# Kernel tuning notes

Hardware: AMD Instinct MI355X
Metric: run time of the kernel (lower is better)

Reference implementation:

```python
import jax, jax.numpy as jnp
import numpy as np

EPS = 1e-6


def _dwconv3x3(x, k):
    # x: [B,C,H,W], k: [C,1,3,3] depthwise kernel (OIHW with feature_group_count=C)
    return jax.lax.conv_general_dilated(
        x, k, window_strides=(1, 1), padding='SAME',
        dimension_numbers=('NCHW', 'OIHW', 'NCHW'),
        feature_group_count=x.shape[1])


def setup_inputs() -> dict:
    key = jax.random.key(0)
    ks = jax.random.split(key, 10)
    B, C, H, W, E = 8, 128, 128, 128, 4
    s = 0.02
    return {
        'x': jax.random.normal(ks[0], (B, C, H, W), jnp.float32),
        'prompt': jax.random.normal(ks[1], (B, C), jnp.float32),
        'gamma': jnp.ones((C,), jnp.float32),
        'beta': jnp.zeros((C,), jnp.float32),
        'rw': jax.random.normal(ks[2], (2 * C, E), jnp.float32) * s,
        'rb': jnp.zeros((E,), jnp.float32),
        'w1': jax.random.normal(ks[3], (E, C, C), jnp.float32) * s,
        'b1': jnp.zeros((E, C), jnp.float32),
        'dw': jax.random.normal(ks[4], (E, C, 1, 3, 3), jnp.float32) * s,
        'bdw': jnp.zeros((E, C), jnp.float32),
        'w2': jax.random.normal(ks[5], (E, C, C), jnp.float32) * s,
        'b2': jnp.zeros((E, C), jnp.float32),
        'pw': jax.random.normal(ks[6], (C, C), jnp.float32) * s,
        'pb': jnp.zeros((C,), jnp.float32),
    }


def reference(x, prompt, gamma, beta, rw, rb, w1, b1, dw, bdw, w2, b2, pw, pb):
    B, C, H, W = x.shape
    E = rb.shape[0]
    topk = 2

    # LayerNorm over channel dim (applied on last axis after permute in torch)
    mu = x.mean(axis=1, keepdims=True)
    var = x.var(axis=1, keepdims=True)
    x_in = (x - mu) * jax.lax.rsqrt(var + EPS)
    x_in = x_in * gamma[None, :, None, None] + beta[None, :, None, None]

    # Router: global avg pooled feature + prompt -> softmax -> top-k
    feat_avg = x_in.mean(axis=(2, 3))                        # [B,C]
    logits = jnp.concatenate([feat_avg, prompt], axis=1) @ rw + rb  # [B,E]
    probs = jax.nn.softmax(logits, axis=-1)
    weights, indices = jax.lax.top_k(probs, topk)            # [B,topk]

    # Per-sample gate over experts: g[b,e] = sum_k weights[b,k] * (indices[b,k]==e)
    gate = jnp.einsum('bk,bke->be', weights, jax.nn.one_hot(indices, E, dtype=x.dtype))

    # Dense all-expert compute (as in the original masked implementation)
    y = jnp.einsum('bchw,eoc->ebohw', x_in, w1) + b1[:, None, :, None, None]  # [E,B,C,H,W]
    y = jax.vmap(_dwconv3x3, in_axes=(0, 0))(y, dw) + bdw[:, None, :, None, None]
    y = jax.nn.gelu(y, approximate=False)
    y = jnp.einsum('ebchw,eoc->ebohw', y, w2) + b2[:, None, :, None, None]

    out = jnp.einsum('ebchw,be->bchw', y, gate)
    proj = jnp.einsum('bchw,oc->bohw', out, pw) + pb[None, :, None, None]
    return x + proj
```

## Files before the change

### kernel.cpp

```cpp
#include <hip/hip_runtime.h>
#include <hip/hip_bf16.h>

#define BB 8
#define CC 128
#define HH 128
#define WW 128
#define HW (HH*WW)
#define EE 4
#define EPSL 1e-6f
#define PT1 8
#define LNP 128

typedef __attribute__((ext_vector_type(8))) short bf16x8;
typedef __attribute__((ext_vector_type(4))) float f32x4;

__device__ inline float b2f(unsigned short u){
  union { unsigned int i; float f; } v; v.i = ((unsigned int)u)<<16; return v.f;
}
__device__ inline unsigned short f2b(float f){
  union { float f; unsigned int i; } v; v.f = f;
  unsigned int x = v.i;
  return (unsigned short)((x + 0x7fffu + ((x>>16)&1u)) >> 16);
}
__device__ inline int swz(int px, int cbyte){
  return cbyte ^ ((((px)&7) ^ (((px)>>3)&3)) << 4);
}

__global__ __launch_bounds__(128) void k_ln(
    const float* __restrict__ x, const float* __restrict__ gamma,
    const float* __restrict__ beta, unsigned short* __restrict__ xin) {
  int b = blockIdx.y;
  int p0 = blockIdx.x*LNP;
  int tid = threadIdx.x;
  const float* xb = x + (size_t)b*CC*HW + p0 + tid;
  float s=0.f, s2=0.f;
  for (int c=0;c<CC;c++){ float v = xb[(size_t)c*HW]; s+=v; s2+=v*v; }
  float mu = s*(1.f/CC);
  float var = s2*(1.f/CC) - mu*mu;
  float rs = rsqrtf(var + EPSL);

  __shared__ unsigned short tile[LNP][CC+8];
  for (int c0=0;c0<CC;c0+=8){
    union { bf16x8 v; unsigned short s[8]; } pk;
    #pragma unroll
    for (int j=0;j<8;j++){
      float v = (xb[(size_t)(c0+j)*HW]-mu)*rs*gamma[c0+j]+beta[c0+j];
      pk.s[j]=f2b(v);
    }
    *(bf16x8*)&tile[tid][c0] = pk.v;
  }
  __syncthreads();
  unsigned short* xo = xin + ((size_t)b*HW + p0)*CC;
  #pragma unroll
  for (int it=0; it<16; ++it){
    int i = it*LNP + tid;
    int pr = i>>4, ck = (i&15)*8;
    *(bf16x8*)(xo + (size_t)i*8) = *(bf16x8*)&tile[pr][ck];
  }
}

__global__ __launch_bounds__(256) void k_feat(
    const unsigned short* __restrict__ xin, float* __restrict__ feat_sum) {
  int b = blockIdx.y;
  int g = blockIdx.x;
  int tid = threadIdx.x;
  int cg = (tid & 15) * 8;
  int po = tid >> 4;
  __shared__ float lfeat[CC];
  for (int c=tid;c<CC;c+=256) lfeat[c]=0.f;
  __syncthreads();
  const unsigned short* base = xin + ((size_t)b*HW + (size_t)g*128)*CC + cg;
  float acc[8] = {};
  #pragma unroll
  for (int i=0;i<8;i++){
    bf16x8 v = *(const bf16x8*)(base + (size_t)(i*16+po)*CC);
    #pragma unroll
    for (int j=0;j<8;j++) acc[j] += b2f((unsigned short)v[j]);
  }
  #pragma unroll
  for (int j=0;j<8;j++) atomicAdd(&lfeat[cg+j], acc[j]);
  __syncthreads();
  if (tid < CC) atomicAdd(&feat_sum[b*CC+tid], lfeat[tid]);
}

__global__ __launch_bounds__(256) void k_router(
    const float* __restrict__ feat_sum, const float* __restrict__ prompt,
    const float* __restrict__ rw, const float* __restrict__ rb,
    const float* __restrict__ b2, const float* __restrict__ pw,
    const float* __restrict__ pb,
    int* __restrict__ eidx, float* __restrict__ wgt, float* __restrict__ bias_out) {
  __shared__ float logits[BB][EE];
  __shared__ float gate[BB][EE];
  __shared__ float cb[BB][CC];
  int t = threadIdx.x;
  if (t < BB*EE) {
    int b = t/EE, e = t%EE;
    float acc = rb[e];
    for (int c=0;c<CC;c++) acc += (feat_sum[b*CC+c]*(1.f/HW))*rw[c*EE+e];
    for (int c=0;c<CC;c++) acc += prompt[b*CC+c]*rw[(CC+c)*EE+e];
    logits[b][e]=acc;
  }
  __syncthreads();
  if (t < BB) {
    int b=t;
    float m=-1e30f;
    for(int e=0;e<EE;e++) m=fmaxf(m,logits[b][e]);
    float s=0.f, pr[EE];
    for(int e=0;e<EE;e++){ pr[e]=__expf(logits[b][e]-m); s+=pr[e]; }
    for(int e=0;e<EE;e++){ pr[e]/=s; gate[b][e]=0.f; }
    int i1=0; for(int e=1;e<EE;e++) if (pr[e]>pr[i1]) i1=e;
    int i2=-1; for(int e=0;e<EE;e++){ if(e==i1) continue; if(i2<0||pr[e]>pr[i2]) i2=e; }
    eidx[b*2]=i1; eidx[b*2+1]=i2;
    wgt[b*2]=pr[i1]; wgt[b*2+1]=pr[i2];
    gate[b][i1]=pr[i1]; gate[b][i2]=pr[i2];
  }
  __syncthreads();
  for (int i=t;i<BB*CC;i+=256){
    int b=i/CC, c=i%CC;
    float a=0.f;
    for(int e=0;e<EE;e++) a += gate[b][e]*b2[e*CC+c];
    cb[b][c]=a;
  }
  __syncthreads();
  for (int i=t;i<BB*CC;i+=256){
    int b=i/CC, o=i%CC;
    float a=pb[o];
    for (int c=0;c<CC;c++) a += pw[o*CC+c]*cb[b][c];
    bias_out[b*CC+o]=a;
  }
}

__global__ __launch_bounds__(128) void k_prep(
    const float* __restrict__ pw, const float* __restrict__ w2,
    const float* __restrict__ w1,
    unsigned short* __restrict__ w2p, unsigned short* __restrict__ w1b){
  int eo = blockIdx.x; int e = eo/CC, o = eo%CC;
  int c = threadIdx.x;
  float a=0.f;
  for (int m=0;m<CC;m++) a += pw[o*CC+m]*w2[((size_t)e*CC+m)*CC+c];
  w2p[((size_t)e*CC+o)*CC+c] = f2b(a);
  w1b[((size_t)e*CC+o)*CC+c] = f2b(w1[((size_t)e*CC+o)*CC+c]);
}

__global__ __launch_bounds__(256) void k_scalew2(
    const unsigned short* __restrict__ w2p, const int* __restrict__ eidx,
    const float* __restrict__ wgt, unsigned short* __restrict__ w2s){
  int bk = blockIdx.y;
  int e = eidx[bk]; float wv = wgt[bk];
  int i = blockIdx.x*256 + threadIdx.x;
  const unsigned short* src = w2p + (size_t)e*CC*CC;
  w2s[(size_t)bk*CC*CC + i] = f2b(wv * b2f(src[i]));
}

__global__ __launch_bounds__(256) void k_gemm1(
    const unsigned short* __restrict__ xin, const unsigned short* __restrict__ w1b,
    const float* __restrict__ b1, const int* __restrict__ eidx,
    unsigned short* __restrict__ t1) {
  int bk = blockIdx.y; int b = bk>>1; int e = eidx[bk];
  int wave = threadIdx.x>>6, lane = threadIdx.x&63;
  int lr = lane&15, lg = lane>>4;
  int ob = wave*32;
  const unsigned short* Ae = w1b + (size_t)e*CC*CC;
  bf16x8 A[2][4];
  #pragma unroll
  for (int of=0; of<2; of++)
    #pragma unroll
    for (int k0=0; k0<4; k0++)
      A[of][k0] = *(const bf16x8*)(Ae + (size_t)(ob+of*16+lr)*CC + k0*32 + lg*8);
  float bs[2][4];
  #pragma unroll
  for (int of=0; of<2; of++)
    #pragma unroll
    for (int r=0; r<4; r++)
      bs[of][r] = b1[e*CC + ob + of*16 + lg*4 + r];

  int p_start = blockIdx.x * (32*PT1);
  const unsigned short* Xb = xin + ((size_t)b*HW + p_start)*CC;
  unsigned short* T = t1 + ((size_t)bk*HW + p_start)*CC;

  bf16x8 Ba[2][4], Bb[2][4];
  auto loadB = [&](bf16x8 (&Bf)[2][4], int tt){
    const unsigned short* Xt = Xb + (size_t)tt*32*CC;
    #pragma unroll
    for (int pf=0; pf<2; pf++)
      #pragma unroll
      for (int k0=0; k0<4; k0++)
        Bf[pf][k0] = *(const bf16x8*)(Xt + (size_t)(pf*16+lr)*CC + k0*32 + lg*8);
  };
  auto comp = [&](bf16x8 (&Bf)[2][4], int tt){
    f32x4 acc[2][2];
    #pragma unroll
    for (int of=0; of<2; of++){ acc[of][0]=(f32x4){0,0,0,0}; acc[of][1]=(f32x4){0,0,0,0}; }
    #pragma unroll
    for (int k0=0; k0<4; k0++)
      #pragma unroll
      for (int of=0; of<2; of++)
        #pragma unroll
        for (int pf=0; pf<2; pf++)
          acc[of][pf] = __builtin_amdgcn_mfma_f32_16x16x32_bf16(A[of][k0], Bf[pf][k0], acc[of][pf],0,0,0);
    unsigned short* Tt = T + (size_t)tt*32*CC;
    #pragma unroll
    for (int of=0; of<2; of++){
      int o0 = ob + of*16 + lg*4;
      #pragma unroll
      for (int pf=0; pf<2; pf++){
        union { unsigned long long u; unsigned short s[4]; } pk;
        #pragma unroll
        for (int r=0; r<4; r++) pk.s[r]=f2b(acc[of][pf][r]+bs[of][r]);
        *(unsigned long long*)(Tt + (size_t)(pf*16+lr)*CC + o0) = pk.u;
      }
    }
  };

  loadB(Ba, 0);
  #pragma unroll
  for (int t=0; t<PT1; t++){
    if ((t&1)==0){ if (t+1<PT1) loadB(Bb, t+1); comp(Ba, t); }
    else         { if (t+1<PT1) loadB(Ba, t+1); comp(Bb, t); }
  }
}

__global__ __launch_bounds__(256) void k_dwg2(
    const unsigned short* __restrict__ t1, const float* __restrict__ dw,
    const float* __restrict__ bdw, const int* __restrict__ eidx,
    const unsigned short* __restrict__ w2s, const float* __restrict__ bias_out,
    const float* __restrict__ x, float* __restrict__ out) {
  int b = blockIdx.y;
  int h = blockIdx.x;
  int tid = threadIdx.x;

  __shared__ unsigned short t3s[2][HH*CC/HH*CC/CC];
  __shared__ unsigned short tile2[2][128*CC];
  __shared__ float skd2[2][CC*9];
  __shared__ float sbd2[2][CC];
  (void)t3s;

  int e0 = eidx[b*2], e1 = eidx[b*2+1];
  for (int i=tid; i<2*CC*9; i+=256){
    int kk = i/(CC*9), j = i%(CC*9);
    skd2[kk][j] = dw[(size_t)(kk? e1:e0)*CC*9 + j];
  }
  for (int i=tid; i<2*CC; i+=256){
    int kk = i/CC, j = i%CC;
    sbd2[kk][j] = bdw[(kk? e1:e0)*CC + j];
  }
  __syncthreads();

  int cg = (tid & 15) * 8;
  int ws = (tid >> 4) * 8;

  #pragma unroll
  for (int kk=0; kk<2; kk++){
    float acc[8][8];
    #pragma unroll
    for (int px=0; px<8; px++)
      #pragma unroll
      for (int j=0; j<8; j++) acc[px][j] = sbd2[kk][cg+j];

    const unsigned short* rowbase = t1 + ((size_t)(b*2+kk)*HW + (size_t)h*WW)*CC + cg;
    #pragma unroll
    for (int dy=0; dy<3; dy++){
      int h2 = h + dy - 1;
      if (h2 < 0 || h2 >= HH) continue;
      const unsigned short* rp = rowbase + (size_t)(dy-1)*WW*CC;
      bf16x8 v[10];
      #pragma unroll
      for (int t=0; t<10; t++){
        int wc = ws + t - 1;
        if (wc >= 0 && wc < WW) v[t] = *(const bf16x8*)(rp + (size_t)wc*CC);
        else                    v[t] = (bf16x8){0,0,0,0,0,0,0,0};
      }
      #pragma unroll
      for (int dx=0; dx<3; dx++){
        float wk[8];
        #pragma unroll
        for (int j=0; j<8; j++) wk[j] = skd2[kk][(cg+j)*9 + dy*3 + dx];
        #pragma unroll
        for (int px=0; px<8; px++)
          #pragma unroll
          for (int j=0; j<8; j++)
            acc[px][j] += b2f((unsigned short)v[px+dx][j]) * wk[j];
      }
    }
    #pragma unroll
    for (int px=0; px<8; px++){
      union { bf16x8 v; unsigned short s[8]; } pk;
      #pragma unroll
      for (int j=0; j<8; j++){
        float a = acc[px][j];
        pk.s[j] = f2b(0.5f*a*(1.f+erff(a*0.70710678f)));
      }
      int p = ws + px;
      *(bf16x8*)((char*)&tile2[kk][0] + p*256 + swz(p, cg*2)) = pk.v;
    }
  }

  int wave = tid>>6, lane = tid&63;
  int lr = lane&15, lg = lane>>4;
  int ob = wave*32;
  bf16x8 A[2][2][4];
  #pragma unroll
  for (int kk=0; kk<2; kk++){
    const unsigned short* Ae = w2s + (size_t)(b*2+kk)*CC*CC;
    #pragma unroll
    for (int of=0; of<2; of++)
      #pragma unroll
      for (int k0=0; k0<4; k0++)
        A[kk][of][k0] = *(const bf16x8*)(Ae + (size_t)(ob+of*16+lr)*CC + k0*32 + lg*8);
  }
  float bo[2][4];
  #pragma unroll
  for (int of=0; of<2; of++)
    #pragma unroll
    for (int r=0; r<4; r++)
      bo[of][r] = bias_out[b*CC + ob + of*16 + lg*4 + r];

  __syncthreads();

  const float* xb = x + (size_t)b*CC*HW + (size_t)h*WW;
  float* obp = out + (size_t)b*CC*HW + (size_t)h*WW;

  #pragma unroll
  for (int tt=0; tt<4; tt++){
    f32x4 acc[2][2];
    #pragma unroll
    for (int of=0; of<2; of++){ acc[of][0]=(f32x4){0,0,0,0}; acc[of][1]=(f32x4){0,0,0,0}; }
    #pragma unroll
    for (int kk=0; kk<2; kk++){
      #pragma unroll
      for (int k0=0; k0<4; k0++){
        int cb = k0*64 + lg*16;
        bf16x8 B0 = *(bf16x8*)((char*)&tile2[kk][0] + (tt*32+lr   )*256 + swz(tt*32+lr,    cb));
        bf16x8 B1 = *(bf16x8*)((char*)&tile2[kk][0] + (tt*32+16+lr)*256 + swz(tt*32+16+lr, cb));
        #pragma unroll
        for (int of=0; of<2; of++){
          acc[of][0] = __builtin_amdgcn_mfma_f32_16x16x32_bf16(A[kk][of][k0], B0, acc[of][0],0,0,0);
          acc[of][1] = __builtin_amdgcn_mfma_f32_16x16x32_bf16(A[kk][of][k0], B1, acc[of][1],0,0,0);
        }
      }
    }
    #pragma unroll
    for (int of=0; of<2; of++){
      int o0 = ob + of*16 + lg*4;
      #pragma unroll
      for (int r=0; r<4; r++){
        #pragma unroll
        for (int pf=0; pf<2; pf++){
          size_t idx = (size_t)(o0+r)*HW + tt*32 + pf*16 + lr;
          obp[idx] = xb[idx] + acc[of][pf][r] + bo[of][r];
        }
      }
    }
  }
}

extern "C" void kernel_launch(void* const* d_in, const int* in_sizes, int n_in,
                              void* d_out, int out_size, void* d_ws, size_t ws_size,
                              hipStream_t stream) {
  const float* x      = (const float*)d_in[0];
  const float* prompt = (const float*)d_in[1];
  const float* gamma  = (const float*)d_in[2];
  const float* beta   = (const float*)d_in[3];
  const float* rw     = (const float*)d_in[4];
  const float* rb     = (const float*)d_in[5];
  const float* w1     = (const float*)d_in[6];
  const float* b1     = (const float*)d_in[7];
  const float* dw     = (const float*)d_in[8];
  const float* bdw    = (const float*)d_in[9];
  const float* w2     = (const float*)d_in[10];
  const float* b2     = (const float*)d_in[11];
  const float* pw     = (const float*)d_in[12];
  const float* pb     = (const float*)d_in[13];
  float* out = (float*)d_out;

  char* base = (char*)d_ws;
  size_t off = 0;
  auto alloc = [&](size_t bytes)->void* {
    void* p = base + off;
    off = (off + bytes + 255) & ~(size_t)255;
    return p;
  };
  unsigned short* xin  = (unsigned short*)alloc((size_t)BB*HW*CC*2);
  unsigned short* t1   = (unsigned short*)alloc((size_t)BB*2*HW*CC*2);
  unsigned short* w1b  = (unsigned short*)alloc((size_t)EE*CC*CC*2);
  unsigned short* w2p  = (unsigned short*)alloc((size_t)EE*CC*CC*2);
  unsigned short* w2s  = (unsigned short*)alloc((size_t)BB*2*CC*CC*2);
  float* feat_sum      = (float*)alloc(BB*CC*4);
  int*   eidx          = (int*)alloc(BB*2*4);
  float* wgt           = (float*)alloc(BB*2*4);
  float* bias_out      = (float*)alloc(BB*CC*4);

  hipMemsetAsync(feat_sum, 0, BB*CC*4, stream);

  k_ln<<<dim3(HW/LNP, BB), LNP, 0, stream>>>(x, gamma, beta, xin);
  k_feat<<<dim3(128, BB), 256, 0, stream>>>(xin, feat_sum);
  k_prep<<<dim3(EE*CC), 128, 0, stream>>>(pw, w2, w1, w2p, w1b);
  k_router<<<dim3(1), 256, 0, stream>>>(feat_sum, prompt, rw, rb, b2, pw, pb,
                                        eidx, wgt, bias_out);
  k_scalew2<<<dim3(CC*CC/256, BB*2), 256, 0, stream>>>(w2p, eidx, wgt, w2s);
  k_gemm1<<<dim3(HW/(32*PT1), BB*2), 256, 0, stream>>>(xin, w1b, b1, eidx, t1);
  k_dwg2<<<dim3(HH, BB), 256, 0, stream>>>(t1, dw, bdw, eidx, w2s, bias_out, x, out);
}
```

Before: 326.5 us.

## Fuse channel-mean pooling into LayerNorm and split dwconv/GEMM2 into halves

The pooled-feature reduction now runs inside the LayerNorm kernel, reading the bf16 tile already in shared memory. This removes the separate k_feat launch and its re-read of xin from global memory. The depthwise-conv plus second-GEMM kernel now processes each image row in two 64-pixel halves, halving the LDS staging tile and the register accumulators per thread, which may allow higher occupancy. In exchange it adds two extra barriers per row, and the neighbouring pixels at each half boundary are loaded twice.

Result: slower. 339.8 us (+4.1%).

```diff
diff --git a/kernel.cpp b/kernel.cpp
--- a/kernel.cpp
+++ b/kernel.cpp
@@ -28,7 +28,8 @@
 
 __global__ __launch_bounds__(128) void k_ln(
     const float* __restrict__ x, const float* __restrict__ gamma,
-    const float* __restrict__ beta, unsigned short* __restrict__ xin) {
+    const float* __restrict__ beta, unsigned short* __restrict__ xin,
+    float* __restrict__ feat_sum) {
   int b = blockIdx.y;
   int p0 = blockIdx.x*LNP;
   int tid = threadIdx.x;
@@ -40,6 +41,8 @@
   float rs = rsqrtf(var + EPSL);
 
   __shared__ unsigned short tile[LNP][CC+8];
+  __shared__ float lfeat[CC];
+  if (tid < CC) lfeat[tid]=0.f;
   for (int c0=0;c0<CC;c0+=8){
     union { bf16x8 v; unsigned short s[8]; } pk;
     #pragma unroll
@@ -57,28 +60,18 @@
     int pr = i>>4, ck = (i&15)*8;
     *(bf16x8*)(xo + (size_t)i*8) = *(bf16x8*)&tile[pr][ck];
   }
-}
-
-__global__ __launch_bounds__(256) void k_feat(
-    const unsigned short* __restrict__ xin, float* __restrict__ feat_sum) {
-  int b = blockIdx.y;
-  int g = blockIdx.x;
-  int tid = threadIdx.x;
   int cg = (tid & 15) * 8;
   int po = tid >> 4;
-  __shared__ float lfeat[CC];
-  for (int c=tid;c<CC;c+=256) lfeat[c]=0.f;
-  __syncthreads();
-  const unsigned short* base = xin + ((size_t)b*HW + (size_t)g*128)*CC + cg;
-  float acc[8] = {};
-  #pragma unroll
-  for (int i=0;i<8;i++){
-    bf16x8 v = *(const bf16x8*)(base + (size_t)(i*16+po)*CC);
-    #pragma unroll
-    for (int j=0;j<8;j++) acc[j] += b2f((unsigned short)v[j]);
-  }
-  #pragma unroll
-  for (int j=0;j<8;j++) atomicAdd(&lfeat[cg+j], acc[j]);
+  float fa[8] = {};
+  #pragma unroll
+  for (int i=0;i<16;i++){
+    int px = i*8 + po;
+    bf16x8 v = *(bf16x8*)&tile[px][cg];
+    #pragma unroll
+    for (int j=0;j<8;j++) fa[j] += b2f((unsigned short)v[j]);
+  }
+  #pragma unroll
+  for (int j=0;j<8;j++) atomicAdd(&lfeat[cg+j], fa[j]);
   __syncthreads();
   if (tid < CC) atomicAdd(&feat_sum[b*CC+tid], lfeat[tid]);
 }
@@ -229,11 +222,9 @@
   int h = blockIdx.x;
   int tid = threadIdx.x;
 
-  __shared__ unsigned short t3s[2][HH*CC/HH*CC/CC];
-  __shared__ unsigned short tile2[2][128*CC];
+  __shared__ unsigned short tile2[2][64*CC];
   __shared__ float skd2[2][CC*9];
   __shared__ float sbd2[2][CC];
-  (void)t3s;
 
   int e0 = eidx[b*2], e1 = eidx[b*2+1];
   for (int i=tid; i<2*CC*9; i+=256){
@@ -244,56 +235,6 @@
     int kk = i/CC, j = i%CC;
     sbd2[kk][j] = bdw[(kk? e1:e0)*CC + j];
   }
-  __syncthreads();
-
-  int cg = (tid & 15) * 8;
-  int ws = (tid >> 4) * 8;
-
-  #pragma unroll
-  for (int kk=0; kk<2; kk++){
-    float acc[8][8];
-    #pragma unroll
-    for (int px=0; px<8; px++)
-      #pragma unroll
-      for (int j=0; j<8; j++) acc[px][j] = sbd2[kk][cg+j];
-
-    const unsigned short* rowbase = t1 + ((size_t)(b*2+kk)*HW + (size_t)h*WW)*CC + cg;
-    #pragma unroll
-    for (int dy=0; dy<3; dy++){
-      int h2 = h + dy - 1;
-      if (h2 < 0 || h2 >= HH) continue;
-      const unsigned short* rp = rowbase + (size_t)(dy-1)*WW*CC;
-      bf16x8 v[10];
-      #pragma unroll
-      for (int t=0; t<10; t++){
-        int wc = ws + t - 1;
-        if (wc >= 0 && wc < WW) v[t] = *(const bf16x8*)(rp + (size_t)wc*CC);
-        else                    v[t] = (bf16x8){0,0,0,0,0,0,0,0};
-      }
-      #pragma unroll
-      for (int dx=0; dx<3; dx++){
-        float wk[8];
-        #pragma unroll
-        for (int j=0; j<8; j++) wk[j] = skd2[kk][(cg+j)*9 + dy*3 + dx];
-        #pragma unroll
-        for (int px=0; px<8; px++)
-          #pragma unroll
-          for (int j=0; j<8; j++)
-            acc[px][j] += b2f((unsigned short)v[px+dx][j]) * wk[j];
-      }
-    }
-    #pragma unroll
-    for (int px=0; px<8; px++){
-      union { bf16x8 v; unsigned short s[8]; } pk;
-      #pragma unroll
-      for (int j=0; j<8; j++){
-        float a = acc[px][j];
-        pk.s[j] = f2b(0.5f*a*(1.f+erff(a*0.70710678f)));
-      }
-      int p = ws + px;
-      *(bf16x8*)((char*)&tile2[kk][0] + p*256 + swz(p, cg*2)) = pk.v;
-    }
-  }
 
   int wave = tid>>6, lane = tid&63;
   int lr = lane&15, lg = lane>>4;
@@ -317,40 +258,93 @@
 
   __syncthreads();
 
+  int cg = (tid & 15) * 8;
+  int slot = tid >> 4;
   const float* xb = x + (size_t)b*CC*HW + (size_t)h*WW;
   float* obp = out + (size_t)b*CC*HW + (size_t)h*WW;
 
   #pragma unroll
-  for (int tt=0; tt<4; tt++){
-    f32x4 acc[2][2];
-    #pragma unroll
-    for (int of=0; of<2; of++){ acc[of][0]=(f32x4){0,0,0,0}; acc[of][1]=(f32x4){0,0,0,0}; }
+  for (int half=0; half<2; half++){
+    int pbase = half*64;
     #pragma unroll
     for (int kk=0; kk<2; kk++){
-      #pragma unroll
-      for (int k0=0; k0<4; k0++){
-        int cb = k0*64 + lg*16;
-        bf16x8 B0 = *(bf16x8*)((char*)&tile2[kk][0] + (tt*32+lr   )*256 + swz(tt*32+lr,    cb));
-        bf16x8 B1 = *(bf16x8*)((char*)&tile2[kk][0] + (tt*32+16+lr)*256 + swz(tt*32+16+lr, cb));
-        #pragma unroll
-        for (int of=0; of<2; of++){
-          acc[of][0] = __builtin_amdgcn_mfma_f32_16x16x32_bf16(A[kk][of][k0], B0, acc[of][0],0,0,0);
-          acc[of][1] = __builtin_amdgcn_mfma_f32_16x16x32_bf16(A[kk][of][k0], B1, acc[of][1],0,0,0);
-        }
+      float acc[4][8];
+      #pragma unroll
+      for (int i=0;i<4;i++)
+        #pragma unroll
+        for (int j=0;j<8;j++) acc[i][j] = sbd2[kk][cg+j];
+      const unsigned short* rowbase = t1 + ((size_t)(b*2+kk)*HW + (size_t)h*WW)*CC + cg;
+      #pragma unroll
+      for (int dy=0; dy<3; dy++){
+        int h2 = h + dy - 1;
+        if (h2 < 0 || h2 >= HH) continue;
+        const unsigned short* rp = rowbase + (size_t)(dy-1)*WW*CC;
+        bf16x8 v[6];
+        #pragma unroll
+        for (int t=0; t<6; t++){
+          int wc = pbase + slot*4 + t - 1;
+          if (wc >= 0 && wc < WW) v[t] = *(const bf16x8*)(rp + (size_t)wc*CC);
+          else                    v[t] = (bf16x8){0,0,0,0,0,0,0,0};
+        }
+        #pragma unroll
+        for (int dx=0; dx<3; dx++){
+          float wk[8];
+          #pragma unroll
+          for (int j=0; j<8; j++) wk[j] = skd2[kk][(cg+j)*9 + dy*3 + dx];
+          #pragma unroll
+          for (int i=0; i<4; i++)
+            #pragma unroll
+            for (int j=0; j<8; j++)
+              acc[i][j] += b2f((unsigned short)v[i+dx][j]) * wk[j];
+        }
+      }
+      #pragma unroll
+      for (int i=0; i<4; i++){
+        union { bf16x8 v; unsigned short s[8]; } pk;
+        #pragma unroll
+        for (int j=0; j<8; j++){
+          float a = acc[i][j];
+          pk.s[j] = f2b(0.5f*a*(1.f+erff(a*0.70710678f)));
+        }
+        int p = slot*4 + i;
+        *(bf16x8*)((char*)&tile2[kk][0] + p*256 + swz(p, cg*2)) = pk.v;
       }
     }
-    #pragma unroll
-    for (int of=0; of<2; of++){
-      int o0 = ob + of*16 + lg*4;
-      #pragma unroll
-      for (int r=0; r<4; r++){
-        #pragma unroll
-        for (int pf=0; pf<2; pf++){
-          size_t idx = (size_t)(o0+r)*HW + tt*32 + pf*16 + lr;
-          obp[idx] = xb[idx] + acc[of][pf][r] + bo[of][r];
+    __syncthreads();
+    #pragma unroll
+    for (int ttl=0; ttl<2; ttl++){
+      f32x4 acc2[2][2];
+      #pragma unroll
+      for (int of=0; of<2; of++){ acc2[of][0]=(f32x4){0,0,0,0}; acc2[of][1]=(f32x4){0,0,0,0}; }
+      #pragma unroll
+      for (int kk=0; kk<2; kk++){
+        #pragma unroll
+        for (int k0=0; k0<4; k0++){
+          int cb = k0*64 + lg*16;
+          int r0 = ttl*32 + lr, r1 = ttl*32 + 16 + lr;
+          bf16x8 B0 = *(bf16x8*)((char*)&tile2[kk][0] + r0*256 + swz(r0, cb));
+          bf16x8 B1 = *(bf16x8*)((char*)&tile2[kk][0] + r1*256 + swz(r1, cb));
+          #pragma unroll
+          for (int of=0; of<2; of++){
+            acc2[of][0] = __builtin_amdgcn_mfma_f32_16x16x32_bf16(A[kk][of][k0], B0, acc2[of][0],0,0,0);
+            acc2[of][1] = __builtin_amdgcn_mfma_f32_16x16x32_bf16(A[kk][of][k0], B1, acc2[of][1],0,0,0);
+          }
+        }
+      }
+      #pragma unroll
+      for (int of=0; of<2; of++){
+        int o0 = ob + of*16 + lg*4;
+        #pragma unroll
+        for (int r=0; r<4; r++){
+          #pragma unroll
+          for (int pf=0; pf<2; pf++){
+            size_t idx = (size_t)(o0+r)*HW + pbase + ttl*32 + pf*16 + lr;
+            obp[idx] = xb[idx] + acc2[of][pf][r] + bo[of][r];
+          }
         }
       }
     }
+    __syncthreads();
   }
 }
 
@@ -392,8 +386,7 @@
 
   hipMemsetAsync(feat_sum, 0, BB*CC*4, stream);
 
-  k_ln<<<dim3(HW/LNP, BB), LNP, 0, stream>>>(x, gamma, beta, xin);
-  k_feat<<<dim3(128, BB), 256, 0, stream>>>(xin, feat_sum);
+  k_ln<<<dim3(HW/LNP, BB), LNP, 0, stream>>>(x, gamma, beta, xin, feat_sum);
   k_prep<<<dim3(EE*CC), 128, 0, stream>>>(pw, w2, w1, w2p, w1b);
   k_router<<<dim3(1), 256, 0, stream>>>(feat_sum, prompt, rw, rb, b2, pw, pb,
                                         eidx, wgt, bias_out);
```
